# Performance work log

Hardware: AMD Instinct MI355X
Metric: run time of the kernel (lower is better)

Reference implementation:

```python
import jax, jax.numpy as jnp
import numpy as np

N = 100000   # nodes
E = 1000000  # edges per graph (avg degree 10)
D = 300      # feature dim


def _layernorm(x, gamma, beta, eps=1e-5):
    mu = jnp.mean(x, axis=-1, keepdims=True)
    var = jnp.mean(jnp.square(x - mu), axis=-1, keepdims=True)
    return (x - mu) * jax.lax.rsqrt(var + eps) * gamma + beta


def _graph_conv(edges, x, W, b, num_nodes):
    # DGL GraphConv with norm='both' and relu activation:
    # h = relu( D_in^{-1/2} A D_out^{-1/2} x W + b )
    src, dst = edges[0], edges[1]
    ones = jnp.ones((edges.shape[1],), x.dtype)
    out_deg = jax.ops.segment_sum(ones, src, num_segments=num_nodes)
    in_deg = jax.ops.segment_sum(ones, dst, num_segments=num_nodes)
    norm_src = jnp.where(out_deg > 0, jax.lax.rsqrt(jnp.maximum(out_deg, 1.0)), 0.0)
    norm_dst = jnp.where(in_deg > 0, jax.lax.rsqrt(jnp.maximum(in_deg, 1.0)), 0.0)
    h = x * norm_src[:, None]                                  # [N, D]
    agg = jax.ops.segment_sum(h[src], dst, num_segments=num_nodes)  # gather+scatter
    agg = agg * norm_dst[:, None]
    return jax.nn.relu(agg @ W + b)


def setup_inputs() -> dict:
    key = jax.random.key(0)
    ks = jax.random.split(key, 8)
    s = 0.05  # weight scale
    return {
        "table_feat": jax.random.normal(ks[0], (N, D), jnp.float32),
        "row_edges": jax.random.randint(ks[1], (2, E), 0, N, jnp.int32),
        "col_edges": jax.random.randint(ks[2], (2, E), 0, N, jnp.int32),
        "Wr": jax.random.normal(ks[3], (D, D), jnp.float32) * s,
        "br": jnp.zeros((D,), jnp.float32),
        "Wc": jax.random.normal(ks[4], (D, D), jnp.float32) * s,
        "bc": jnp.zeros((D,), jnp.float32),
        "Wrs": jax.random.normal(ks[5], (D, D), jnp.float32) * s,
        "brs": jnp.zeros((D,), jnp.float32),
        "g_rs": jnp.ones((D,), jnp.float32),
        "b_rs": jnp.zeros((D,), jnp.float32),
        "Wcs": jax.random.normal(ks[6], (D, D), jnp.float32) * s,
        "bcs": jnp.zeros((D,), jnp.float32),
        "g_cs": jnp.ones((D,), jnp.float32),
        "b_cs": jnp.zeros((D,), jnp.float32),
        "Wm": jax.random.normal(ks[7], (2 * D, D), jnp.float32) * s,
        "bm": jnp.zeros((D,), jnp.float32),
        "g_m": jnp.ones((D,), jnp.float32),
        "b_m": jnp.zeros((D,), jnp.float32),
    }


def reference(table_feat, row_edges, col_edges, Wr, br, Wc, bc,
              Wrs, brs, g_rs, b_rs, Wcs, bcs, g_cs, b_cs,
              Wm, bm, g_m, b_m):
    rowg = _graph_conv(row_edges, table_feat, Wr, br, N)   # row_aware GraphConv
    colg = _graph_conv(col_edges, table_feat, Wc, bc, N)   # col_aware GraphConv
    rowg = _layernorm(rowg @ Wrs + brs, g_rs, b_rs)        # row_graph_support
    colg = _layernorm(colg @ Wcs + bcs, g_cs, b_cs)        # col_graph_support
    merged = jnp.concatenate([rowg, colg], axis=1)          # [N, 2D]
    return _layernorm(merged @ Wm + bm, g_m, b_m)           # graph_merge
```

## Files before the change

### kernel.cpp

```cpp
#include <hip/hip_runtime.h>
#include <stdint.h>

#define SP 304
#define ASP 312
#define NT 10
#define KS300 19

typedef unsigned short u16;
using short8 = __attribute__((ext_vector_type(8))) short;
using f32x16 = __attribute__((ext_vector_type(16))) float;

__device__ __forceinline__ float b2f(u16 u) {
    return __uint_as_float(((unsigned)u) << 16);
}
__device__ __forceinline__ u16 f2b(float f) {
    unsigned u = __float_as_uint(f);
    return (u16)((u + 0x7FFFu + ((u >> 16) & 1u)) >> 16);
}
__device__ __forceinline__ float scrub(float v) {
    unsigned u = __float_as_uint(v);
    return (((u >> 23) & 0xFFu) == 0xFFu) ? 0.f : v;
}
__device__ __forceinline__ u16 sb16(u16 v) {
    return (((v >> 7) & 0xFFu) == 0xFFu) ? (u16)0 : v;
}

__global__ void detect_dtype(const u16* __restrict__ xs, int* __restrict__ flag) {
    __shared__ int cnt[256];
    int c = 0;
    for (int i = 0; i < 16; i++) {
        u16 v = xs[threadIdx.x * 16 + i];
        unsigned e = (v >> 7) & 0xFFu;
        c += (e >= 100u && e <= 150u) ? 1 : 0;
    }
    cnt[threadIdx.x] = c;
    __syncthreads();
    for (int s = 128; s > 0; s >>= 1) {
        if (threadIdx.x < s) cnt[threadIdx.x] += cnt[threadIdx.x + s];
        __syncthreads();
    }
    if (threadIdx.x == 0) flag[0] = (cnt[0] >= 3686) ? 1 : 0;
}

__global__ __launch_bounds__(256) void conv_x(const void* __restrict__ x, u16* __restrict__ xb,
                                              int total4, const int* __restrict__ flag) {
    const bool BF16 = flag[0] != 0;
    int idx = blockIdx.x * 256 + threadIdx.x;
    if (idx >= total4) return;
    int node = idx / 76, c = idx - node * 76;
    ushort4 v = make_ushort4(0, 0, 0, 0);
    if (c < 75) {
        if (BF16) {
            v = *(const ushort4*)((const u16*)x + (size_t)node * 300 + c * 4);
            v.x = sb16(v.x); v.y = sb16(v.y); v.z = sb16(v.z); v.w = sb16(v.w);
        } else {
            float4 f = *(const float4*)((const float*)x + (size_t)node * 300 + c * 4);
            v = make_ushort4(f2b(scrub(f.x)), f2b(scrub(f.y)), f2b(scrub(f.z)), f2b(scrub(f.w)));
        }
    }
    *(ushort4*)(xb + (size_t)node * SP + c * 4) = v;
}

__global__ void pack_b(const void* __restrict__ W, u16* __restrict__ P, int nseg,
                       const int* __restrict__ flag) {
    const bool BF16 = flag[0] != 0;
    int idx = blockIdx.x * 256 + threadIdx.x;
    int total = nseg * KS300 * NT * 512;
    if (idx >= total) return;
    int j = idx & 7, lane = (idx >> 3) & 63, t = idx >> 9;
    int nt = t % NT, ks = t / NT;
    int seg = ks / KS300, ksl = ks - seg * KS300;
    int kk = ksl * 16 + ((lane >> 5) << 3) + j;
    int n = nt * 32 + (lane & 31);
    u16 v = 0;
    if (kk < 300 && n < 300) {
        int wk = seg * 300 + kk;
        if (BF16) v = sb16(((const u16*)W)[(size_t)wk * 300 + n]);
        else      v = f2b(scrub(((const float*)W)[(size_t)wk * 300 + n]));
    }
    P[idx] = v;
}

__global__ void conv_params(const void* p0, const void* p1, const void* p2, const void* p3,
                            const void* p4, const void* p5, const void* p6, const void* p7,
                            const void* p8, const void* p9, const void* p10,
                            float* __restrict__ pbuf, const int* __restrict__ flag) {
    const bool BF16 = flag[0] != 0;
    int idx = blockIdx.x * 256 + threadIdx.x;
    if (idx >= 11 * 304) return;
    int j = idx / 304, c = idx % 304;
    const void* ps[11] = {p0, p1, p2, p3, p4, p5, p6, p7, p8, p9, p10};
    float v = 0.f;
    if (c < 300) {
        if (BF16) v = b2f(sb16(((const u16*)ps[j])[c]));
        else      v = scrub(((const float*)ps[j])[c]);
    }
    pbuf[j * 304 + c] = v;
}

__global__ void count_deg(const int* __restrict__ src, const int* __restrict__ dst, int E,
                          int* __restrict__ outd, int* __restrict__ ind) {
    int e = blockIdx.x * 256 + threadIdx.x;
    if (e < E) {
        atomicAdd(&outd[src[e]], 1);
        atomicAdd(&ind[dst[e]], 1);
    }
}

__global__ __launch_bounds__(256) void alloc_norm(int Nn,
                           const int* __restrict__ odR, const int* __restrict__ idR,
                           const int* __restrict__ odC, const int* __restrict__ idC,
                           int* __restrict__ offR, int* __restrict__ offC,
                           float* __restrict__ nsR, float* __restrict__ ndR,
                           float* __restrict__ nsC, float* __restrict__ ndC,
                           int* __restrict__ cur2) {
    __shared__ int sR[256], sC[256];
    __shared__ int baseR, baseC;
    int tid = threadIdx.x;
    int i = blockIdx.x * 256 + tid;
    int dR = (i < Nn) ? idR[i] : 0;
    int dC = (i < Nn) ? idC[i] : 0;
    sR[tid] = dR; sC[tid] = dC;
    __syncthreads();
    for (int off = 1; off < 256; off <<= 1) {
        int vR = (tid >= off) ? sR[tid - off] : 0;
        int vC = (tid >= off) ? sC[tid - off] : 0;
        __syncthreads();
        sR[tid] += vR; sC[tid] += vC;
        __syncthreads();
    }
    if (tid == 0) {
        baseR = atomicAdd(&cur2[0], sR[255]);
        baseC = atomicAdd(&cur2[1], sC[255]);
    }
    __syncthreads();
    if (i < Nn) {
        offR[i] = baseR + sR[tid] - dR;
        offC[i] = baseC + sC[tid] - dC;
        nsR[i] = odR[i] > 0 ? rsqrtf((float)odR[i]) : 0.f;
        ndR[i] = idR[i] > 0 ? rsqrtf((float)idR[i]) : 0.f;
        nsC[i] = odC[i] > 0 ? rsqrtf((float)odC[i]) : 0.f;
        ndC[i] = idC[i] > 0 ? rsqrtf((float)idC[i]) : 0.f;
    }
}

__global__ void fill_csr(const int* __restrict__ src, const int* __restrict__ dst, int E,
                         const int* __restrict__ offs, int* __restrict__ cursor,
                         int* __restrict__ adj) {
    int e = blockIdx.x * 256 + threadIdx.x;
    if (e < E) {
        int d = dst[e];
        int p = offs[d] + atomicAdd(&cursor[d], 1);
        adj[p] = src[e];
    }
}

__global__ __launch_bounds__(256) void aggregate(
    const u16* __restrict__ xb, const int* __restrict__ adj, const int* __restrict__ offs,
    const int* __restrict__ deg, const float* __restrict__ ns, const float* __restrict__ nd,
    u16* __restrict__ agg, int Nn) {
    int w = threadIdx.x >> 6, lane = threadIdx.x & 63;
    int node = blockIdx.x * 4 + w;
    if (node >= Nn) return;
    int bg = offs[node], cnt = deg[node];
    const bool part = lane < 12;
    const int c0 = 4 * lane, c1 = 256 + 4 * lane;
    float a0 = 0, a1 = 0, a2 = 0, a3 = 0, p0 = 0, p1 = 0, p2 = 0, p3 = 0;
    int j = 0;
    for (; j + 4 <= cnt; j += 4) {
        int s0 = adj[bg + j], s1 = adj[bg + j + 1], s2 = adj[bg + j + 2], s3 = adj[bg + j + 3];
        float n0 = ns[s0], n1 = ns[s1], n2 = ns[s2], n3 = ns[s3];
        const u16* q0 = xb + (size_t)s0 * SP;
        const u16* q1 = xb + (size_t)s1 * SP;
        const u16* q2 = xb + (size_t)s2 * SP;
        const u16* q3 = xb + (size_t)s3 * SP;
        ushort4 v0 = *(const ushort4*)(q0 + c0);
        ushort4 v1 = *(const ushort4*)(q1 + c0);
        ushort4 v2 = *(const ushort4*)(q2 + c0);
        ushort4 v3 = *(const ushort4*)(q3 + c0);
        a0 += b2f(v0.x) * n0 + b2f(v1.x) * n1 + b2f(v2.x) * n2 + b2f(v3.x) * n3;
        a1 += b2f(v0.y) * n0 + b2f(v1.y) * n1 + b2f(v2.y) * n2 + b2f(v3.y) * n3;
        a2 += b2f(v0.z) * n0 + b2f(v1.z) * n1 + b2f(v2.z) * n2 + b2f(v3.z) * n3;
        a3 += b2f(v0.w) * n0 + b2f(v1.w) * n1 + b2f(v2.w) * n2 + b2f(v3.w) * n3;
        if (part) {
            ushort4 u0 = *(const ushort4*)(q0 + c1);
            ushort4 u1 = *(const ushort4*)(q1 + c1);
            ushort4 u2 = *(const ushort4*)(q2 + c1);
            ushort4 u3 = *(const ushort4*)(q3 + c1);
            p0 += b2f(u0.x) * n0 + b2f(u1.x) * n1 + b2f(u2.x) * n2 + b2f(u3.x) * n3;
            p1 += b2f(u0.y) * n0 + b2f(u1.y) * n1 + b2f(u2.y) * n2 + b2f(u3.y) * n3;
            p2 += b2f(u0.z) * n0 + b2f(u1.z) * n1 + b2f(u2.z) * n2 + b2f(u3.z) * n3;
            p3 += b2f(u0.w) * n0 + b2f(u1.w) * n1 + b2f(u2.w) * n2 + b2f(u3.w) * n3;
        }
    }
    for (; j < cnt; ++j) {
        int s = adj[bg + j];
        float nv = ns[s];
        const u16* rp = xb + (size_t)s * SP;
        ushort4 v = *(const ushort4*)(rp + c0);
        a0 += b2f(v.x) * nv; a1 += b2f(v.y) * nv; a2 += b2f(v.z) * nv; a3 += b2f(v.w) * nv;
        if (part) {
            ushort4 u = *(const ushort4*)(rp + c1);
            p0 += b2f(u.x) * nv; p1 += b2f(u.y) * nv; p2 += b2f(u.z) * nv; p3 += b2f(u.w) * nv;
        }
    }
    float ndv = nd[node];
    u16* o = agg + (size_t)node * SP;
    *(ushort4*)(o + c0) = make_ushort4(f2b(a0 * ndv), f2b(a1 * ndv), f2b(a2 * ndv), f2b(a3 * ndv));
    if (part)
        *(ushort4*)(o + c1) = make_ushort4(f2b(p0 * ndv), f2b(p1 * ndv), f2b(p2 * ndv), f2b(p3 * ndv));
}

__device__ __forceinline__ void stage_a(const u16* __restrict__ A, u16* __restrict__ lds,
                                        int mb, int M, int tid) {
    for (int idx = tid; idx < 64 * 38; idx += 256) {
        int row = idx / 38, ck = idx - row * 38;
        int gr = min(mb + row, M - 1);
        *(short8*)(lds + row * ASP + ck * 8) = *(const short8*)(A + (size_t)gr * SP + ck * 8);
    }
}

#define LDB(dst, blp, ksi)                                                    \
    {                                                                         \
        const u16* _bb = (blp) + (size_t)(ksi) * (NT * 512);                  \
        _Pragma("unroll")                                                     \
        for (int _i = 0; _i < 5; ++_i) dst[_i] = *(const short8*)(_bb + _i * 512); \
    }
#define MM5(af, bf)                                                           \
    {                                                                         \
        _Pragma("unroll")                                                     \
        for (int _i = 0; _i < 5; ++_i)                                        \
            acc[_i] = __builtin_amdgcn_mfma_f32_32x32x16_bf16((af), bf[_i], acc[_i], 0, 0, 0); \
    }
#define GEMM19(arowp, blp, kbase)                                             \
    {                                                                         \
        short8 q0[5], q1[5], q2[5];                                           \
        LDB(q0, blp, (kbase));                                                \
        LDB(q1, blp, (kbase) + 1);                                            \
        LDB(q2, blp, (kbase) + 2);                                            \
        for (int ks = 0; ks < 18; ks += 3) {                                  \
            short8 af0 = *(const short8*)((arowp) + ks * 16);                 \
            MM5(af0, q0);                                                     \
            LDB(q0, blp, (kbase) + min(ks + 3, 18));                          \
            short8 af1 = *(const short8*)((arowp) + (ks + 1) * 16);           \
            MM5(af1, q1);                                                     \
            LDB(q1, blp, (kbase) + min(ks + 4, 18));                          \
            short8 af2 = *(const short8*)((arowp) + (ks + 2) * 16);           \
            MM5(af2, q2);                                                     \
            LDB(q2, blp, (kbase) + min(ks + 5, 18));                          \
        }                                                                     \
        short8 aft = *(const short8*)((arowp) + 18 * 16);                     \
        MM5(aft, q0);                                                         \
    }

__global__ __launch_bounds__(256, 3) void gemm_fused(
    const u16* __restrict__ Ain, const u16* __restrict__ B1p, const u16* __restrict__ B2p,
    const float* __restrict__ bias1, const float* __restrict__ bias2,
    const float* __restrict__ gamma2, const float* __restrict__ beta2,
    u16* __restrict__ outp, int M) {
    __shared__ __align__(16) char smem[2048 + 64 * ASP * 2];
    float* red = (float*)smem;
    u16* hb = (u16*)(smem + 2048);

    const int tid = threadIdx.x;
    const int w = tid >> 6, l = tid & 63;
    const int pr = w >> 1, sd = w & 1;
    const int mb = blockIdx.x * 64;
    const int r0 = mb + pr * 32;
    const bool act = r0 < M;
    const int lc = l & 31, hi = l >> 5;
    const u16* bl1 = B1p + (size_t)(sd * 5) * 512 + (size_t)l * 8;
    const u16* bl2 = B2p + (size_t)(sd * 5) * 512 + (size_t)l * 8;
    const int colbase = sd * 160;
    const u16* arow = hb + (size_t)(pr * 32 + lc) * ASP + hi * 8;

    stage_a(Ain, hb, mb, M, tid);
    __syncthreads();

    f32x16 acc[5];
#pragma unroll
    for (int i = 0; i < 5; ++i)
#pragma unroll
        for (int r = 0; r < 16; ++r) acc[i][r] = 0.f;

    GEMM19(arow, bl1, 0);
    __syncthreads();

    if (act) {
#pragma unroll
        for (int i = 0; i < 5; ++i) {
            int col = colbase + i * 32 + lc;
            if (col < 304) {
                float bb = col < 300 ? bias1[col] : 0.f;
#pragma unroll
                for (int r = 0; r < 16; ++r) {
                    int rowl = 4 * hi + (r & 3) + 8 * (r >> 2);
                    float v = scrub(acc[i][r] + bb);
                    v = v > 0.f ? v : 0.f;
                    hb[(size_t)(pr * 32 + rowl) * ASP + col] = col < 300 ? f2b(v) : (u16)0;
                }
            }
        }
    }
    __syncthreads();

#pragma unroll
    for (int i = 0; i < 5; ++i)
#pragma unroll
        for (int r = 0; r < 16; ++r) acc[i][r] = 0.f;
    GEMM19(arow, bl2, 0);

    float sum[16], ssq[16];
#pragma unroll
    for (int r = 0; r < 16; ++r) { sum[r] = 0.f; ssq[r] = 0.f; }
#pragma unroll
    for (int i = 0; i < 5; ++i) {
        int col = colbase + i * 32 + lc;
        bool cv = col < 300;
        float bb = cv ? bias2[col] : 0.f;
#pragma unroll
        for (int r = 0; r < 16; ++r) {
            float v = cv ? scrub(acc[i][r] + bb) : 0.f;
            acc[i][r] = v;
            sum[r] += v;
            ssq[r] += v * v;
        }
    }
#pragma unroll
    for (int off = 1; off < 32; off <<= 1) {
#pragma unroll
        for (int r = 0; r < 16; ++r) {
            sum[r] += __shfl_xor(sum[r], off);
            ssq[r] += __shfl_xor(ssq[r], off);
        }
    }
    if (act) {
#pragma unroll
        for (int r = 0; r < 16; ++r) {
            if (lc == r) {
                int rowl = 4 * hi + (r & 3) + 8 * (r >> 2);
                float* q = red + ((pr * 2 + sd) * 32 + rowl) * 2;
                q[0] = sum[r]; q[1] = ssq[r];
            }
        }
    }
    __syncthreads();
    float mean[16], inv[16];
    if (act) {
#pragma unroll
        for (int r = 0; r < 16; ++r) {
            int rowl = 4 * hi + (r & 3) + 8 * (r >> 2);
            const float* q = red + ((pr * 2 + (1 - sd)) * 32 + rowl) * 2;
            float s = sum[r] + q[0], qq = ssq[r] + q[1];
            mean[r] = s * (1.f / 300.f);
            float var = fmaxf(qq * (1.f / 300.f) - mean[r] * mean[r], 0.f);
            inv[r] = rsqrtf(var + 1e-5f);
        }
    }

    u16* stg = hb;
    if (act) {
#pragma unroll
        for (int i = 0; i < 5; ++i) {
            int col = colbase + i * 32 + lc;
            if (col < 304) {
                float g = col < 300 ? gamma2[col] : 0.f;
                float be = col < 300 ? beta2[col] : 0.f;
#pragma unroll
                for (int r = 0; r < 16; ++r) {
                    int rowl = 4 * hi + (r & 3) + 8 * (r >> 2);
                    float v = (acc[i][r] - mean[r]) * inv[r] * g + be;
                    stg[(size_t)(pr * 32 + rowl) * SP + col] = col < 300 ? f2b(v) : (u16)0;
                }
            }
        }
    }
    __syncthreads();
    int rows = min(64, M - mb);
    u16* dst = outp + (size_t)mb * SP;
    if (rows == 64) {
#pragma unroll
        for (int k = 0; k < 10; ++k) {
            int idx = k * 256 + tid;
            if (idx < 2432) *(short8*)(dst + idx * 8) = *(const short8*)(stg + idx * 8);
        }
    } else {
        for (int idx = tid; idx < rows * SP; idx += 256) dst[idx] = stg[idx];
    }
}

__global__ __launch_bounds__(256, 3) void gemm_merge(
    const u16* __restrict__ A1, const u16* __restrict__ A2,
    const u16* __restrict__ Bp, const float* __restrict__ bias,
    const float* __restrict__ gamma, const float* __restrict__ beta,
    void* __restrict__ out, int M, const int* __restrict__ flag) {
    const bool f32out = (flag[0] == 0);
    __shared__ __align__(16) char smem[2048 + 64 * ASP * 2];
    float* red = (float*)smem;
    u16* hb = (u16*)(smem + 2048);

    const int tid = threadIdx.x;
    const int w = tid >> 6, l = tid & 63;
    const int pr = w >> 1, sd = w & 1;
    const int mb = blockIdx.x * 64;
    const int r0 = mb + pr * 32;
    const bool act = r0 < M;
    const int lc = l & 31, hi = l >> 5;
    const u16* bl = Bp + (size_t)(sd * 5) * 512 + (size_t)l * 8;
    const int colbase = sd * 160;
    const u16* arow = hb + (size_t)(pr * 32 + lc) * ASP + hi * 8;

    f32x16 acc[5];
#pragma unroll
    for (int i = 0; i < 5; ++i)
#pragma unroll
        for (int r = 0; r < 16; ++r) acc[i][r] = 0.f;

    stage_a(A1, hb, mb, M, tid);
    __syncthreads();
    GEMM19(arow, bl, 0);
    __syncthreads();
    stage_a(A2, hb, mb, M, tid);
    __syncthreads();
    GEMM19(arow, bl, KS300);

    float sum[16], ssq[16];
#pragma unroll
    for (int r = 0; r < 16; ++r) { sum[r] = 0.f; ssq[r] = 0.f; }
#pragma unroll
    for (int i = 0; i < 5; ++i) {
        int col = colbase + i * 32 + lc;
        bool cv = col < 300;
        float bb = cv ? bias[col] : 0.f;
#pragma unroll
        for (int r = 0; r < 16; ++r) {
            float v = cv ? scrub(acc[i][r] + bb) : 0.f;
            acc[i][r] = v;
            sum[r] += v;
            ssq[r] += v * v;
        }
    }
#pragma unroll
    for (int off = 1; off < 32; off <<= 1) {
#pragma unroll
        for (int r = 0; r < 16; ++r) {
            sum[r] += __shfl_xor(sum[r], off);
            ssq[r] += __shfl_xor(ssq[r], off);
        }
    }
    if (act) {
#pragma unroll
        for (int r = 0; r < 16; ++r) {
            if (lc == r) {
                int rowl = 4 * hi + (r & 3) + 8 * (r >> 2);
                float* q = red + ((pr * 2 + sd) * 32 + rowl) * 2;
                q[0] = sum[r]; q[1] = ssq[r];
            }
        }
    }
    __syncthreads();
    float mean[16], inv[16];
    if (act) {
#pragma unroll
        for (int r = 0; r < 16; ++r) {
            int rowl = 4 * hi + (r & 3) + 8 * (r >> 2);
            const float* q = red + ((pr * 2 + (1 - sd)) * 32 + rowl) * 2;
            float s = sum[r] + q[0], qq = ssq[r] + q[1];
            mean[r] = s * (1.f / 300.f);
            float var = fmaxf(qq * (1.f / 300.f) - mean[r] * mean[r], 0.f);
            inv[r] = rsqrtf(var + 1e-5f);
        }
    }

    if (!f32out) {
        u16* stg = hb;
        if (act) {
#pragma unroll
            for (int i = 0; i < 5; ++i) {
                int col = colbase + i * 32 + lc;
                if (col < 300) {
                    float g = gamma[col], be = beta[col];
#pragma unroll
                    for (int r = 0; r < 16; ++r) {
                        int rowl = 4 * hi + (r & 3) + 8 * (r >> 2);
                        float v = (acc[i][r] - mean[r]) * inv[r] * g + be;
                        stg[(pr * 32 + rowl) * 300 + col] = f2b(v);
                    }
                }
            }
        }
        __syncthreads();
        int rows = min(64, M - mb);
        u16* dst = (u16*)out + (size_t)mb * 300;
        if (rows == 64) {
#pragma unroll
            for (int k = 0; k < 10; ++k) {
                int idx = k * 256 + tid;
                if (idx < 2400) *(short8*)(dst + idx * 8) = *(const short8*)(stg + idx * 8);
            }
        } else {
            for (int idx = tid; idx < rows * 300; idx += 256) dst[idx] = stg[idx];
        }
    } else {
        float* fst = (float*)hb;
        for (int pp = 0; pp < 2; ++pp) {
            __syncthreads();
            if (pr == pp && act) {
#pragma unroll
                for (int i = 0; i < 5; ++i) {
                    int col = colbase + i * 32 + lc;
                    if (col < 300) {
                        float g = gamma[col], be = beta[col];
#pragma unroll
                        for (int r = 0; r < 16; ++r) {
                            int rowl = 4 * hi + (r & 3) + 8 * (r >> 2);
                            float v = (acc[i][r] - mean[r]) * inv[r] * g + be;
                            fst[rowl * 300 + col] = v;
                        }
                    }
                }
            }
            __syncthreads();
            int tr0 = mb + pp * 32;
            if (tr0 < M) {
                int rows = min(32, M - tr0);
                float* dst = (float*)out + (size_t)tr0 * 300;
                if (rows == 32) {
#pragma unroll
                    for (int k = 0; k < 10; ++k) {
                        int idx = k * 256 + tid;
                        if (idx < 2400) *(float4*)(dst + idx * 4) = *(const float4*)(fst + idx * 4);
                    }
                } else {
                    for (int idx = tid; idx < rows * 300; idx += 256) dst[idx] = fst[idx];
                }
            }
        }
    }
}

extern "C" void kernel_launch(void* const* d_in, const int* in_sizes, int n_in,
                              void* d_out, int out_size, void* d_ws, size_t ws_size,
                              hipStream_t stream) {
    (void)n_in; (void)out_size; (void)ws_size;
    const void* x   = d_in[0];
    const int* re   = (const int*)d_in[1];
    const int* ce   = (const int*)d_in[2];

    const int Nn = in_sizes[0] / 300;
    const int Er = in_sizes[1] / 2;
    const int Ec = in_sizes[2] / 2;

    char* p = (char*)d_ws;
    size_t off = 0;
    auto balloc = [&](size_t bytes) -> void* {
        void* r = p + off;
        off += (bytes + 255) & ~(size_t)255;
        return r;
    };
    int* degR  = (int*)balloc((size_t)Nn * 4);
    int* odegR = (int*)balloc((size_t)Nn * 4);
    int* degC  = (int*)balloc((size_t)Nn * 4);
    int* odegC = (int*)balloc((size_t)Nn * 4);
    int* curR  = (int*)balloc((size_t)Nn * 4);
    int* curC  = (int*)balloc((size_t)Nn * 4);
    int* cur2  = (int*)balloc(64 * 4);
    size_t zbytes = off;
    int* flag  = (int*)balloc(256);
    int* offsR = (int*)balloc((size_t)Nn * 4);
    int* offsC = (int*)balloc((size_t)Nn * 4);
    float* nsR = (float*)balloc((size_t)Nn * 4);
    float* ndR = (float*)balloc((size_t)Nn * 4);
    float* nsC = (float*)balloc((size_t)Nn * 4);
    float* ndC = (float*)balloc((size_t)Nn * 4);
    int* adjR  = (int*)balloc((size_t)Er * 4);
    int* adjC  = (int*)balloc((size_t)Ec * 4);
    const size_t PB1 = (size_t)KS300 * NT * 512;
    u16* WrP   = (u16*)balloc(PB1 * 2);
    u16* WcP   = (u16*)balloc(PB1 * 2);
    u16* WrsP  = (u16*)balloc(PB1 * 2);
    u16* WcsP  = (u16*)balloc(PB1 * 2);
    u16* WmP   = (u16*)balloc(2 * PB1 * 2);
    float* pbuf = (float*)balloc(11 * 304 * 4);
    u16* xb    = (u16*)balloc((size_t)Nn * SP * 2);
    u16* B2    = (u16*)balloc((size_t)Nn * SP * 2);
    u16* B3    = (u16*)balloc((size_t)Nn * SP * 2);

    const float* pbr  = pbuf + 0 * 304;
    const float* pbc  = pbuf + 1 * 304;
    const float* pbrs = pbuf + 2 * 304;
    const float* pgrs = pbuf + 3 * 304;
    const float* pBrs = pbuf + 4 * 304;
    const float* pbcs = pbuf + 5 * 304;
    const float* pgcs = pbuf + 6 * 304;
    const float* pBcs = pbuf + 7 * 304;
    const float* pbm  = pbuf + 8 * 304;
    const float* pgm  = pbuf + 9 * 304;
    const float* pBm  = pbuf + 10 * 304;

    detect_dtype<<<1, 256, 0, stream>>>((const u16*)x, flag);
    hipMemsetAsync(d_ws, 0, zbytes, stream);

    const int total4 = Nn * 76;
    conv_x<<<(total4 + 255) / 256, 256, 0, stream>>>(x, xb, total4, flag);

#define PK(Wsrc, Pdst, nseg)                                                                  \
    pack_b<<<(int)(((nseg) * PB1 + 255) / 256), 256, 0, stream>>>(Wsrc, Pdst, nseg, flag)
    PK(d_in[3], WrP, 1);
    PK(d_in[5], WcP, 1);
    PK(d_in[7], WrsP, 1);
    PK(d_in[11], WcsP, 1);
    PK(d_in[15], WmP, 2);
#undef PK

    conv_params<<<14, 256, 0, stream>>>(d_in[4], d_in[6], d_in[8], d_in[9], d_in[10],
                                        d_in[12], d_in[13], d_in[14], d_in[16], d_in[17],
                                        d_in[18], pbuf, flag);

    count_deg<<<(Er + 255) / 256, 256, 0, stream>>>(re, re + Er, Er, odegR, degR);
    count_deg<<<(Ec + 255) / 256, 256, 0, stream>>>(ce, ce + Ec, Ec, odegC, degC);
    alloc_norm<<<(Nn + 255) / 256, 256, 0, stream>>>(Nn, odegR, degR, odegC, degC,
                                                     offsR, offsC, nsR, ndR, nsC, ndC, cur2);
    fill_csr<<<(Er + 255) / 256, 256, 0, stream>>>(re, re + Er, Er, offsR, curR, adjR);
    fill_csr<<<(Ec + 255) / 256, 256, 0, stream>>>(ce, ce + Ec, Ec, offsC, curC, adjC);

    aggregate<<<(Nn + 3) / 4, 256, 0, stream>>>(xb, adjR, offsR, degR, nsR, ndR, B2, Nn);
    aggregate<<<(Nn + 3) / 4, 256, 0, stream>>>(xb, adjC, offsC, degC, nsC, ndC, B3, Nn);

    const int gb = (Nn + 63) / 64;
    gemm_fused<<<gb, 256, 0, stream>>>(B2, WrP, WrsP, pbr, pbrs, pgrs, pBrs, B2, Nn);
    gemm_fused<<<gb, 256, 0, stream>>>(B3, WcP, WcsP, pbc, pbcs, pgcs, pBcs, B3, Nn);
    gemm_merge<<<gb, 256, 0, stream>>>(B2, B3, WmP, pbm, pgm, pBm, d_out, Nn, flag);
}
```

Before: 1.100 ms.

## Privatize degree counters into 8 groups and merge graph-setup launches

Degree counting and CSR filling now spread atomics across 8 private copies of the per-node counters, selected by block index, to reduce atomic contention. The per-group prefix offsets are computed in the normalization kernel, which also resets the in-degree counters so they can be reused as fill cursors. The row and column graphs are processed in single fused launches, and the five weight-packing launches collapse into one. This costs 8x larger counter arrays (the per-group offsets are placed in scratch space inside B3) and more memory traffic in alloc_norm2.

```diff
diff --git a/kernel.cpp b/kernel.cpp
--- a/kernel.cpp
+++ b/kernel.cpp
@@ -5,6 +5,7 @@
 #define ASP 312
 #define NT 10
 #define KS300 19
+#define NGRP 8
 
 typedef unsigned short u16;
 using short8 = __attribute__((ext_vector_type(8))) short;
@@ -61,16 +62,20 @@
     *(ushort4*)(xb + (size_t)node * SP + c * 4) = v;
 }
 
-__global__ void pack_b(const void* __restrict__ W, u16* __restrict__ P, int nseg,
-                       const int* __restrict__ flag) {
+__global__ void pack_all(const void* __restrict__ w0, const void* __restrict__ w1,
+                         const void* __restrict__ w2, const void* __restrict__ w3,
+                         const void* __restrict__ w4,
+                         u16* __restrict__ P, const int* __restrict__ flag) {
     const bool BF16 = flag[0] != 0;
+    const int PB1i = KS300 * NT * 512;
     int idx = blockIdx.x * 256 + threadIdx.x;
-    int total = nseg * KS300 * NT * 512;
-    if (idx >= total) return;
-    int j = idx & 7, lane = (idx >> 3) & 63, t = idx >> 9;
+    if (idx >= 6 * PB1i) return;
+    int u = idx / PB1i, r = idx - u * PB1i;
+    const void* W = (u == 0) ? w0 : (u == 1) ? w1 : (u == 2) ? w2 : (u == 3) ? w3 : w4;
+    int seg = (u < 4) ? 0 : (u - 4);
+    int j = r & 7, lane = (r >> 3) & 63, t = r >> 9;
     int nt = t % NT, ks = t / NT;
-    int seg = ks / KS300, ksl = ks - seg * KS300;
-    int kk = ksl * 16 + ((lane >> 5) << 3) + j;
+    int kk = ks * 16 + ((lane >> 5) << 3) + j;
     int n = nt * 32 + (lane & 31);
     u16 v = 0;
     if (kk < 300 && n < 300) {
@@ -98,19 +103,28 @@
     pbuf[j * 304 + c] = v;
 }
 
-__global__ void count_deg(const int* __restrict__ src, const int* __restrict__ dst, int E,
-                          int* __restrict__ outd, int* __restrict__ ind) {
+__global__ void count2(const int* __restrict__ rS, const int* __restrict__ rD, int Er,
+                       const int* __restrict__ cS, const int* __restrict__ cD, int Ec,
+                       int* __restrict__ od8R, int* __restrict__ id8R,
+                       int* __restrict__ od8C, int* __restrict__ id8C, int Nn) {
     int e = blockIdx.x * 256 + threadIdx.x;
-    if (e < E) {
-        atomicAdd(&outd[src[e]], 1);
-        atomicAdd(&ind[dst[e]], 1);
-    }
-}
-
-__global__ __launch_bounds__(256) void alloc_norm(int Nn,
-                           const int* __restrict__ odR, const int* __restrict__ idR,
-                           const int* __restrict__ odC, const int* __restrict__ idC,
-                           int* __restrict__ offR, int* __restrict__ offC,
+    int base = (blockIdx.x & (NGRP - 1)) * Nn;
+    if (e < Er) {
+        atomicAdd(&od8R[base + rS[e]], 1);
+        atomicAdd(&id8R[base + rD[e]], 1);
+    }
+    if (e < Ec) {
+        atomicAdd(&od8C[base + cS[e]], 1);
+        atomicAdd(&id8C[base + cD[e]], 1);
+    }
+}
+
+__global__ __launch_bounds__(256) void alloc_norm2(int Nn,
+                           int* __restrict__ od8R, int* __restrict__ id8R,
+                           int* __restrict__ od8C, int* __restrict__ id8C,
+                           int* __restrict__ offsR, int* __restrict__ offsC,
+                           int* __restrict__ off8R, int* __restrict__ off8C,
+                           int* __restrict__ degR, int* __restrict__ degC,
                            float* __restrict__ nsR, float* __restrict__ ndR,
                            float* __restrict__ nsC, float* __restrict__ ndC,
                            int* __restrict__ cur2) {
@@ -118,9 +132,18 @@
     __shared__ int baseR, baseC;
     int tid = threadIdx.x;
     int i = blockIdx.x * 256 + tid;
-    int dR = (i < Nn) ? idR[i] : 0;
-    int dC = (i < Nn) ? idC[i] : 0;
-    sR[tid] = dR; sC[tid] = dC;
+    int idr[NGRP], idc[NGRP];
+    int odRt = 0, idRt = 0, odCt = 0, idCt = 0;
+    if (i < Nn) {
+#pragma unroll
+        for (int g = 0; g < NGRP; ++g) {
+            odRt += od8R[g * Nn + i];
+            idr[g] = id8R[g * Nn + i]; idRt += idr[g];
+            odCt += od8C[g * Nn + i];
+            idc[g] = id8C[g * Nn + i]; idCt += idc[g];
+        }
+    }
+    sR[tid] = idRt; sC[tid] = idCt;
     __syncthreads();
     for (int off = 1; off < 256; off <<= 1) {
         int vR = (tid >= off) ? sR[tid - off] : 0;
@@ -135,23 +158,39 @@
     }
     __syncthreads();
     if (i < Nn) {
-        offR[i] = baseR + sR[tid] - dR;
-        offC[i] = baseC + sC[tid] - dC;
-        nsR[i] = odR[i] > 0 ? rsqrtf((float)odR[i]) : 0.f;
-        ndR[i] = idR[i] > 0 ? rsqrtf((float)idR[i]) : 0.f;
-        nsC[i] = odC[i] > 0 ? rsqrtf((float)odC[i]) : 0.f;
-        ndC[i] = idC[i] > 0 ? rsqrtf((float)idC[i]) : 0.f;
-    }
-}
-
-__global__ void fill_csr(const int* __restrict__ src, const int* __restrict__ dst, int E,
-                         const int* __restrict__ offs, int* __restrict__ cursor,
-                         int* __restrict__ adj) {
+        int oR = baseR + sR[tid] - idRt;
+        int oC = baseC + sC[tid] - idCt;
+        offsR[i] = oR; offsC[i] = oC;
+        degR[i] = idRt; degC[i] = idCt;
+        int pR = oR, pC = oC;
+#pragma unroll
+        for (int g = 0; g < NGRP; ++g) {
+            off8R[g * Nn + i] = pR; pR += idr[g]; id8R[g * Nn + i] = 0;
+            off8C[g * Nn + i] = pC; pC += idc[g]; id8C[g * Nn + i] = 0;
+        }
+        nsR[i] = odRt > 0 ? rsqrtf((float)odRt) : 0.f;
+        ndR[i] = idRt > 0 ? rsqrtf((float)idRt) : 0.f;
+        nsC[i] = odCt > 0 ? rsqrtf((float)odCt) : 0.f;
+        ndC[i] = idCt > 0 ? rsqrtf((float)idCt) : 0.f;
+    }
+}
+
+__global__ void fill2(const int* __restrict__ rS, const int* __restrict__ rD, int Er,
+                      const int* __restrict__ cS, const int* __restrict__ cD, int Ec,
+                      const int* __restrict__ off8R, int* __restrict__ cur8R, int* __restrict__ adjR,
+                      const int* __restrict__ off8C, int* __restrict__ cur8C, int* __restrict__ adjC,
+                      int Nn) {
     int e = blockIdx.x * 256 + threadIdx.x;
-    if (e < E) {
-        int d = dst[e];
-        int p = offs[d] + atomicAdd(&cursor[d], 1);
-        adj[p] = src[e];
+    int base = (blockIdx.x & (NGRP - 1)) * Nn;
+    if (e < Er) {
+        int d = rD[e];
+        int p = off8R[base + d] + atomicAdd(&cur8R[base + d], 1);
+        adjR[p] = rS[e];
+    }
+    if (e < Ec) {
+        int d = cD[e];
+        int p = off8C[base + d] + atomicAdd(&cur8C[base + d], 1);
+        adjC[p] = cS[e];
     }
 }
 
@@ -558,17 +597,17 @@
         off += (bytes + 255) & ~(size_t)255;
         return r;
     };
-    int* degR  = (int*)balloc((size_t)Nn * 4);
-    int* odegR = (int*)balloc((size_t)Nn * 4);
-    int* degC  = (int*)balloc((size_t)Nn * 4);
-    int* odegC = (int*)balloc((size_t)Nn * 4);
-    int* curR  = (int*)balloc((size_t)Nn * 4);
-    int* curC  = (int*)balloc((size_t)Nn * 4);
-    int* cur2  = (int*)balloc(64 * 4);
+    int* od8R = (int*)balloc((size_t)NGRP * Nn * 4);
+    int* id8R = (int*)balloc((size_t)NGRP * Nn * 4);
+    int* od8C = (int*)balloc((size_t)NGRP * Nn * 4);
+    int* id8C = (int*)balloc((size_t)NGRP * Nn * 4);
+    int* cur2 = (int*)balloc(64 * 4);
     size_t zbytes = off;
     int* flag  = (int*)balloc(256);
     int* offsR = (int*)balloc((size_t)Nn * 4);
     int* offsC = (int*)balloc((size_t)Nn * 4);
+    int* degR  = (int*)balloc((size_t)Nn * 4);
+    int* degC  = (int*)balloc((size_t)Nn * 4);
     float* nsR = (float*)balloc((size_t)Nn * 4);
     float* ndR = (float*)balloc((size_t)Nn * 4);
     float* nsC = (float*)balloc((size_t)Nn * 4);
@@ -576,15 +615,18 @@
     int* adjR  = (int*)balloc((size_t)Er * 4);
     int* adjC  = (int*)balloc((size_t)Ec * 4);
     const size_t PB1 = (size_t)KS300 * NT * 512;
-    u16* WrP   = (u16*)balloc(PB1 * 2);
-    u16* WcP   = (u16*)balloc(PB1 * 2);
-    u16* WrsP  = (u16*)balloc(PB1 * 2);
-    u16* WcsP  = (u16*)balloc(PB1 * 2);
-    u16* WmP   = (u16*)balloc(2 * PB1 * 2);
+    u16* Wpack = (u16*)balloc(6 * PB1 * 2);
+    u16* WrP  = Wpack;
+    u16* WcP  = Wpack + PB1;
+    u16* WrsP = Wpack + 2 * PB1;
+    u16* WcsP = Wpack + 3 * PB1;
+    u16* WmP  = Wpack + 4 * PB1;
     float* pbuf = (float*)balloc(11 * 304 * 4);
     u16* xb    = (u16*)balloc((size_t)Nn * SP * 2);
     u16* B2    = (u16*)balloc((size_t)Nn * SP * 2);
     u16* B3    = (u16*)balloc((size_t)Nn * SP * 2);
+    int* off8R = (int*)B3;
+    int* off8C = (int*)(B3 + (size_t)NGRP * Nn * 2);
 
     const float* pbr  = pbuf + 0 * 304;
     const float* pbc  = pbuf + 1 * 304;
@@ -604,25 +646,22 @@
     const int total4 = Nn * 76;
     conv_x<<<(total4 + 255) / 256, 256, 0, stream>>>(x, xb, total4, flag);
 
-#define PK(Wsrc, Pdst, nseg)                                                                  \
-    pack_b<<<(int)(((nseg) * PB1 + 255) / 256), 256, 0, stream>>>(Wsrc, Pdst, nseg, flag)
-    PK(d_in[3], WrP, 1);
-    PK(d_in[5], WcP, 1);
-    PK(d_in[7], WrsP, 1);
-    PK(d_in[11], WcsP, 1);
-    PK(d_in[15], WmP, 2);
-#undef PK
+    pack_all<<<(int)((6 * PB1 + 255) / 256), 256, 0, stream>>>(
+        d_in[3], d_in[5], d_in[7], d_in[11], d_in[15], Wpack, flag);
 
     conv_params<<<14, 256, 0, stream>>>(d_in[4], d_in[6], d_in[8], d_in[9], d_in[10],
                                         d_in[12], d_in[13], d_in[14], d_in[16], d_in[17],
                                         d_in[18], pbuf, flag);
 
-    count_deg<<<(Er + 255) / 256, 256, 0, stream>>>(re, re + Er, Er, odegR, degR);
-    count_deg<<<(Ec + 255) / 256, 256, 0, stream>>>(ce, ce + Ec, Ec, odegC, degC);
-    alloc_norm<<<(Nn + 255) / 256, 256, 0, stream>>>(Nn, odegR, degR, odegC, degC,
-                                                     offsR, offsC, nsR, ndR, nsC, ndC, cur2);
-    fill_csr<<<(Er + 255) / 256, 256, 0, stream>>>(re, re + Er, Er, offsR, curR, adjR);
-    fill_csr<<<(Ec + 255) / 256, 256, 0, stream>>>(ce, ce + Ec, Ec, offsC, curC, adjC);
+    const int Emax = Er > Ec ? Er : Ec;
+    const int EB = (Emax + 255) / 256;
+    count2<<<EB, 256, 0, stream>>>(re, re + Er, Er, ce, ce + Ec, Ec,
+                                   od8R, id8R, od8C, id8C, Nn);
+    alloc_norm2<<<(Nn + 255) / 256, 256, 0, stream>>>(Nn, od8R, id8R, od8C, id8C,
+                                                      offsR, offsC, off8R, off8C,
+                                                      degR, degC, nsR, ndR, nsC, ndC, cur2);
+    fill2<<<EB, 256, 0, stream>>>(re, re + Er, Er, ce, ce + Ec, Ec,
+                                  off8R, id8R, adjR, off8C, id8C, adjC, Nn);
 
     aggregate<<<(Nn + 3) / 4, 256, 0, stream>>>(xb, adjR, offsR, degR, nsR, ndR, B2, Nn);
     aggregate<<<(Nn + 3) / 4, 256, 0, stream>>>(xb, adjC, offsC, degC, nsC, ndC, B3, Nn);
```

Measured after the change: 1.090 ms. Within noise of the previous version (-0.9%).
